# Kernel optimization log

Measured on AMD Instinct MI355X. Metric: run time of the kernel, lower is better.

The kernel has to match this reference:

```python
import jax, jax.numpy as jnp
import numpy as np

B, S, D, H, NS = 4, 4096, 1024, 16, 128
DA, DF = 512, 4096
DK, DV = DA // H, D // H  # 32, 64
TEMP = 1.0
EPS = 1e-6


def setup_inputs() -> dict:
    key = jax.random.key(0)
    ks = jax.random.split(key, 8)
    r = lambda k, shp: jax.random.normal(k, shp, jnp.float32) * 0.02
    return dict(
        x=jax.random.normal(ks[0], (B, S, D), jnp.float32),
        mask=jnp.ones((B, S), jnp.float32),
        residual_scale=jnp.ones((1,), jnp.float32),
        w_q=r(ks[1], (D, DA)), b_q=jnp.zeros((DA,), jnp.float32),
        w_kv=r(ks[2], (D, DA + D)), b_kv=jnp.zeros((DA + D,), jnp.float32),
        w_s=r(ks[3], (D, H * NS)), b_s=jnp.zeros((H * NS,), jnp.float32),
        w_cat=r(ks[4], (D, D)), b_cat=jnp.zeros((D,), jnp.float32),
        norm1_w=jnp.ones((D,), jnp.float32), norm2_w=jnp.ones((D,), jnp.float32),
        w1=r(ks[5], (D, DF)), b1=jnp.zeros((DF,), jnp.float32),
        w2=r(ks[6], (DF, D)), b2=jnp.zeros((D,), jnp.float32),
    )


def _rms(x, w):
    return x * jax.lax.rsqrt(jnp.mean(x * x, axis=-1, keepdims=True) + EPS) * w


def _forward(x, mask, residual_scale, w_q, b_q, w_kv, b_kv, w_s, b_s,
             w_cat, b_cat, norm1_w, norm2_w, w1, b1, w2, b2):
    neg = jnp.finfo(jnp.float32).min
    xn = _rms(x, norm1_w)
    q = (xn @ w_q + b_q).reshape(B, S, H, DK).transpose(0, 2, 1, 3)        # [B,H,S,DK]
    kv = (xn @ w_kv + b_kv).reshape(B, S, H, DK + DV).transpose(0, 2, 1, 3)  # [B,H,S,DK+DV]
    k_raw, v_raw = kv[..., :DK], kv[..., DK:]

    # DSZRC sampler: per-head soft routing of S tokens -> NS sampled KV rows
    logits = (x @ w_s + b_s).reshape(B, S, H, NS).transpose(0, 2, 3, 1)    # [B,H,NS,S]
    logits = jnp.where(mask[:, None, None, :] > 0, logits, neg)
    probs = jax.nn.softmax(logits / TEMP, axis=-1)
    kv_s = jnp.einsum('bhms,bhsd->bhmd', probs, kv)                        # [B,H,NS,DK+DV]
    k_s, v_s = kv_s[..., :DK], kv_s[..., DK:]

    # branch 1: dense SDPA over sampled KV
    scale = 1.0 / np.sqrt(DK).astype(np.float32)
    att = jax.nn.softmax(jnp.einsum('bhqd,bhkd->bhqk', q, k_s) * scale, axis=-1)
    out1 = jnp.einsum('bhqk,bhkd->bhqd', att, v_s)                         # [B,H,S,DV]

    # branch 2: fp16 sliding-window flash attn, left window = NS (keys i-NS..i)
    f16 = lambda t: t.astype(jnp.float16).astype(jnp.float32)
    qh, kh, vh = f16(q), f16(k_raw), f16(v_raw)
    bs = NS
    nb = S // bs
    qb = qh.reshape(B, H, nb, bs, DK)
    kb = kh.reshape(B, H, nb, bs, DK)
    vb = vh.reshape(B, H, nb, bs, DV)
    shift = lambda t: jnp.concatenate([jnp.zeros_like(t[:, :, :1]), t[:, :, :-1]], axis=2)
    kctx = jnp.concatenate([shift(kb), kb], axis=3)                        # [B,H,nb,2bs,DK]
    vctx = jnp.concatenate([shift(vb), vb], axis=3)
    sc = jnp.einsum('bhnad,bhnkd->bhnak', qb, kctx) * scale                # [B,H,nb,bs,2bs]
    a = jnp.arange(bs)[:, None]
    bcol = jnp.arange(2 * bs)[None, :]
    band = (bcol >= a) & (bcol <= a + NS)                                  # 0 <= q-k <= NS
    tpos = jnp.arange(nb)[:, None, None]
    valid = band[None] & ((tpos > 0) | (bcol >= bs)[None])                 # no keys before pos 0
    p = jax.nn.softmax(jnp.where(valid[None, None], sc, neg), axis=-1)
    out2 = f16(jnp.einsum('bhnak,bhnkd->bhnad', p, vctx)).reshape(B, H, S, DV)

    x_att = (out1 + out2).transpose(0, 2, 1, 3).reshape(B, S, D)
    x = x + (x_att @ w_cat + b_cat) * residual_scale
    h = _rms(x, norm2_w)
    x = x + (jax.nn.gelu(h @ w1 + b1, approximate=False) @ w2 + b2) * residual_scale
    return x


def reference(x, mask, residual_scale, w_q, b_q, w_kv, b_kv, w_s, b_s,
              w_cat, b_cat, norm1_w, norm2_w, w1, b1, w2, b2):
    return _forward(x, mask, residual_scale, w_q, b_q, w_kv, b_kv, w_s, b_s,
                    w_cat, b_cat, norm1_w, norm2_w, w1, b1, w2, b2)
```

## Files before the change

kernel.cpp:

```cpp
#include <hip/hip_runtime.h>
#include <cstdint>
#include <cmath>

#define DEV __device__ __forceinline__

using f16 = _Float16;
typedef f16  f16x4 __attribute__((ext_vector_type(4)));
typedef f16  f16x8 __attribute__((ext_vector_type(8)));
typedef float f32x4 __attribute__((ext_vector_type(4)));

constexpr int Bq = 4, Sq = 4096, Hq = 16;
constexpr int Tq = Bq * Sq;

DEV void gload_lds16(const void* g, void* l) {
  __builtin_amdgcn_global_load_lds(
      (const __attribute__((address_space(1))) void*)g,
      (__attribute__((address_space(3))) void*)l, 16, 0, 0);
}

DEV void stage_swz(const char* gbase, long gstride, char* lds, int nbytes,
                   int rowlog, int swzmask) {
  int tid = threadIdx.x;
  for (int b0 = 0; b0 < nbytes; b0 += 4096) {
    int P = b0 + tid * 16;
    int L = P ^ (((P >> rowlog) & swzmask) << 4);
    long row  = L >> rowlog;
    int  colb = L & ((1 << rowlog) - 1);
    gload_lds16(gbase + row * gstride + colb, lds + b0 + (tid & ~63) * 16);
  }
}

DEV void stage_swz512(const char* gbase, long gstride, char* lds, int nbytes,
                      int rowlog, int swzmask) {
  int tid = threadIdx.x;
  for (int b0 = 0; b0 < nbytes; b0 += 8192) {
    int P = b0 + tid * 16;
    int L = P ^ (((P >> rowlog) & swzmask) << 4);
    long row  = L >> rowlog;
    int  colb = L & ((1 << rowlog) - 1);
    gload_lds16(gbase + row * gstride + colb, lds + b0 + (tid & ~63) * 16);
  }
}

DEV float wave16_max(float v) {
#pragma unroll
  for (int d = 1; d < 16; d <<= 1) v = fmaxf(v, __shfl_xor(v, d, 64));
  return v;
}
DEV float wave16_sum(float v) {
#pragma unroll
  for (int d = 1; d < 16; d <<= 1) v += __shfl_xor(v, d, 64);
  return v;
}

__global__ __launch_bounds__(256) void wcast_k(const float* __restrict__ W,
                                               f16* __restrict__ Wt, int K, int N) {
  int n0 = blockIdx.x * 32, k0 = blockIdx.y * 32;
  __shared__ float tile[32][33];
  int tid = threadIdx.x, r = tid >> 5, c = tid & 31;
#pragma unroll
  for (int i = 0; i < 4; ++i)
    tile[r + i * 8][c] = W[(size_t)(k0 + r + i * 8) * N + n0 + c];
  __syncthreads();
#pragma unroll
  for (int i = 0; i < 4; ++i) {
    int rr = r + i * 8;
    Wt[(size_t)(n0 + rr) * K + k0 + c] = (f16)tile[c][rr];
  }
}

__global__ void bias_concat_k(const float* __restrict__ bq, const float* __restrict__ bkv,
                              float* __restrict__ out) {
  int i = blockIdx.x * 256 + threadIdx.x;
  out[i] = (i < 512) ? bq[i] : bkv[i - 512];
}

__global__ __launch_bounds__(256) void rmsnorm_k(const float* __restrict__ x,
                                                 const float* __restrict__ w,
                                                 f16* __restrict__ xn) {
  int row = blockIdx.x, tid = threadIdx.x;
  float4 v = ((const float4*)(x + (size_t)row * 1024))[tid];
  float ss = v.x * v.x + v.y * v.y + v.z * v.z + v.w * v.w;
#pragma unroll
  for (int d = 1; d < 64; d <<= 1) ss += __shfl_xor(ss, d, 64);
  __shared__ float red[4];
  if ((tid & 63) == 0) red[tid >> 6] = ss;
  __syncthreads();
  float tot = red[0] + red[1] + red[2] + red[3];
  float r = rsqrtf(tot * (1.0f / 1024.0f) + 1e-6f);
  float4 wv = ((const float4*)w)[tid];
  f16x4 o;
  o[0] = (f16)(v.x * r * wv.x); o[1] = (f16)(v.y * r * wv.y);
  o[2] = (f16)(v.z * r * wv.z); o[3] = (f16)(v.w * r * wv.w);
  *(f16x4*)(xn + (size_t)row * 1024 + tid * 4) = o;
}

template <int MODE>
__global__ __launch_bounds__(512) void gemm_k(const f16* __restrict__ A, const f16* __restrict__ Bt,
                                              const float* __restrict__ bias,
                                              float* __restrict__ outF, f16* __restrict__ o1,
                                              f16* __restrict__ o2, f16* __restrict__ o3,
                                              const float* __restrict__ resid,
                                              const float* __restrict__ rsp,
                                              int M, int N, int K, int lda, int ldb, int pp) {
  __shared__ alignas(16) char smA[32768];
  __shared__ alignas(16) char smB[32768];
  int nwgx = gridDim.x, nbc = gridDim.y;
  int bidl = blockIdx.y * nwgx + blockIdx.x;
  int cpx = (nwgx * nbc) >> 3;
  int xcd = bidl & 7, pos = bidl >> 3;
  int rpm = cpx / nbc;
  int nbi = pos / rpm, mbi = pos % rpm;
  int mb = xcd * rpm + mbi;
  long n0 = (long)nbi * 256;
  int tid = threadIdx.x, lane = tid & 63, wv = tid >> 6;
  int wr = wv >> 2, wc = wv & 3;
  long m0;
  long t0 = 0;
  int bq = 0;
  if (MODE == 5) {
    bq = mb >> 3; int sb = mb & 7;
    m0 = (long)sb * 256;
    t0 = (long)bq * 4096 + (long)pp * 2048 + m0;
  } else {
    m0 = (long)mb * 256;
  }
  f32x4 acc[8][4] = {};
  const char* Ab = (MODE == 5 || MODE == 7) ? nullptr : (const char*)(A + m0 * lda);
  const char* Bb = (const char*)(Bt + n0 * ldb);

  for (int k0 = 0; k0 < K; k0 += 64) {
    __syncthreads();
    stage_swz512(Bb + (long)k0 * 2, (long)ldb * 2, smB, 32768, 7, 7);
    if (MODE == 5) {
      int P = tid * 16;
#pragma unroll
      for (int b0 = 0; b0 < 32768; b0 += 8192) {
        int PP = b0 + P;
        int L = PP ^ (((PP >> 7) & 7) << 4);
        int row = L >> 7, colf = (L & 127) >> 1;
        const float* src = resid + (size_t)(t0 + row) * 1024 + k0 + colf;
        float4 u0 = *(const float4*)src;
        float4 u1 = *(const float4*)(src + 4);
        f16x8 o;
        o[0] = (f16)u0.x; o[1] = (f16)u0.y; o[2] = (f16)u0.z; o[3] = (f16)u0.w;
        o[4] = (f16)u1.x; o[5] = (f16)u1.y; o[6] = (f16)u1.z; o[7] = (f16)u1.w;
        *(f16x8*)(smA + PP) = o;
      }
    } else if (MODE == 7) {
      const char* Ab7 = (const char*)(A + (((m0 >> 12) * 16 + (k0 >> 6)) * 4096 + (m0 & 4095)) * 64);
      stage_swz512(Ab7, 128, smA, 32768, 7, 7);
    } else {
      stage_swz512(Ab + (long)k0 * 2, (long)lda * 2, smA, 32768, 7, 7);
    }
    __syncthreads();
#pragma unroll
    for (int kk = 0; kk < 2; ++kk) {
      int kbyte = kk * 64 + (lane >> 4) * 16;
      f16x8 aF[8], bF[4];
#pragma unroll
      for (int m = 0; m < 8; ++m) {
        int L = (wr * 128 + m * 16 + (lane & 15)) * 128 + kbyte;
        aF[m] = *(const f16x8*)(smA + (L ^ (((L >> 7) & 7) << 4)));
      }
#pragma unroll
      for (int n = 0; n < 4; ++n) {
        int L = (wc * 64 + n * 16 + (lane & 15)) * 128 + kbyte;
        bF[n] = *(const f16x8*)(smB + (L ^ (((L >> 7) & 7) << 4)));
      }
#pragma unroll
      for (int m = 0; m < 8; ++m)
#pragma unroll
        for (int n = 0; n < 4; ++n)
          acc[m][n] = __builtin_amdgcn_mfma_f32_16x16x32_f16(aF[m], bF[n], acc[m][n], 0, 0, 0);
    }
  }
  float rsv = (MODE == 2 || MODE == 7) ? rsp[0] : 0.f;
#pragma unroll
  for (int m = 0; m < 8; ++m)
#pragma unroll
    for (int n = 0; n < 4; ++n) {
      long gn = n0 + wc * 64 + n * 16 + (lane & 15);
      float bv = bias[gn];
      long rbase = m0 + wr * 128 + m * 16 + (lane >> 4) * 4;
      if (MODE == 4) {
        long b = rbase >> 12, s = rbase & 4095;
        if (gn < 512) {
          long h = gn >> 5, dk = gn & 31;
#pragma unroll
          for (int i = 0; i < 4; ++i)
            o1[(((size_t)b * 16 + h) * 4096 + s + i) * 32 + dk] = (f16)(acc[m][n][i] + bv);
        } else {
          long c2 = gn - 512, h = c2 / 96, j = c2 % 96;
          if (j < 32) {
#pragma unroll
            for (int i = 0; i < 4; ++i)
              o2[(((size_t)b * 16 + h) * 4096 + s + i) * 32 + j] = (f16)(acc[m][n][i] + bv);
          } else {
            f16x4 pk;
#pragma unroll
            for (int i = 0; i < 4; ++i) pk[i] = (f16)(acc[m][n][i] + bv);
            *(f16x4*)(o3 + (((size_t)b * 16 + h) * 64 + (j - 32)) * 4096 + s) = pk;
          }
        }
      } else {
#pragma unroll
        for (int i = 0; i < 4; ++i) {
          long gm = rbase + i;
          float v = acc[m][n][i] + bv;
          if (MODE == 2 || MODE == 7) {
            long idx = gm * N + gn;
            outF[idx] = resid[idx] + v * rsv;
          } else if (MODE == 3) {
            float u = v * 0.7978845608028654f * (1.f + 0.044715f * v * v);
            float e = __expf(fminf(2.f * u, 80.f));
            o1[gm * N + gn] = (f16)(v * (e / (e + 1.f)));
          } else {
            o1[((size_t)bq * 2048 + gn) * 2048 + gm] = (f16)v;
          }
        }
      }
    }
}

__global__ __launch_bounds__(256) void kvs_k(const f16* __restrict__ lt,
                                             const f16* __restrict__ kh,
                                             const f16* __restrict__ vT,
                                             const float* __restrict__ mask,
                                             float* __restrict__ pacc, int pass) {
  int gx = blockIdx.x, nsb = gx & 3, sc = gx >> 2;
  int h = blockIdx.y, b = blockIdx.z;
  int bh = b * 16 + h;
  __shared__ alignas(16) char smA[4096];
  __shared__ alignas(16) f16 smB[112][88];
  int tid = threadIdx.x, lane = tid & 63, w = tid >> 6;
  int mf = w >> 1, nb0 = (w & 1) * 4, nfr = (w & 1) ? 3 : 4;
  for (int idx = tid; idx < 16 * 64; idx += 256) {
    int r = 96 + (idx >> 6), c2 = idx & 63;
    smB[r][c2] = (r == 96) ? (f16)1.0f : (f16)0.0f;
  }
  f32x4 acc[4] = {};
  const f16* ltb = lt + ((size_t)bh * 128 + nsb * 32) * 2048;
  for (int it = 0; it < 4; ++it) {
    int sl0 = sc * 256 + it * 64;
    int s0g = pass * 2048 + sl0;
    __syncthreads();
    {
      int P = tid * 16;
      int L = P ^ (((P >> 7) & 7) << 4);
      int row = L >> 7, colf = (L & 127) >> 1;
      f16x8 lv = *(const f16x8*)(ltb + (size_t)row * 2048 + sl0 + colf);
      const float* mrow = mask + (size_t)b * 4096 + s0g + colf;
      float4 m0v = *(const float4*)mrow, m1v = *(const float4*)(mrow + 4);
      float mm[8] = {m0v.x, m0v.y, m0v.z, m0v.w, m1v.x, m1v.y, m1v.z, m1v.w};
      f16x8 o;
#pragma unroll
      for (int j = 0; j < 8; ++j)
        o[j] = (f16)((mm[j] > 0.f) ? expf((float)lv[j] - 8.0f) : 0.0f);
      *(f16x8*)(smA + P) = o;
    }
    {
      int sl = tid >> 2, jg = (tid & 3) * 8;
      f16x8 u = *(const f16x8*)(kh + ((size_t)bh * 4096 + s0g + sl) * 32 + jg);
#pragma unroll
      for (int j = 0; j < 8; ++j) smB[jg + j][sl] = u[j];
    }
#pragma unroll
    for (int half = 0; half < 2; ++half) {
      int task = tid + half * 256;
      int dv = task >> 3, sl0v = (task & 7) * 8;
      f16x8 u = *(const f16x8*)(vT + ((size_t)bh * 64 + dv) * 4096 + s0g + sl0v);
      *(f16x8*)(&smB[32 + dv][sl0v]) = u;
    }
    __syncthreads();
#pragma unroll
    for (int kk = 0; kk < 2; ++kk) {
      int kbyte = kk * 64 + (lane >> 4) * 16;
      int L = (mf * 16 + (lane & 15)) * 128 + kbyte;
      f16x8 aF = *(const f16x8*)(smA + (L ^ (((L >> 7) & 7) << 4)));
#pragma unroll
      for (int n = 0; n < 4; ++n)
        if (n < nfr) {
          f16x8 bF = *(const f16x8*)((const char*)smB + ((nb0 + n) * 16 + (lane & 15)) * 176 + kbyte);
          acc[n] = __builtin_amdgcn_mfma_f32_16x16x32_f16(aF, bF, acc[n], 0, 0, 0);
        }
    }
  }
  int slot = pass * 8 + sc;
  float* pb = pacc + (((size_t)bh * 4 + nsb) * 16 + slot) * 3584;
#pragma unroll
  for (int n = 0; n < 4; ++n)
    if (n < nfr) {
      int col = (nb0 + n) * 16 + (lane & 15);
#pragma unroll
      for (int i = 0; i < 4; ++i) {
        int nsrow = mf * 16 + (lane >> 4) * 4 + i;
        pb[(size_t)nsrow * 112 + col] = acc[n][i];
      }
    }
}

__global__ __launch_bounds__(256) void kvs_fin_k(const float* __restrict__ pacc,
                                                 f16* __restrict__ ks, f16* __restrict__ vst) {
  int bh = blockIdx.x, tid = threadIdx.x;
  __shared__ float den[128];
  const float* base = pacc + (size_t)bh * 4 * 16 * 3584;
  if (tid < 128) {
    int nsb = tid >> 5, nsl = tid & 31;
    float d = 0.f;
#pragma unroll
    for (int slot = 0; slot < 16; ++slot)
      d += base[((size_t)nsb * 16 + slot) * 3584 + (size_t)nsl * 112 + 96];
    den[tid] = d;
  }
  __syncthreads();
  for (int e = tid; e < 12288; e += 256) {
    int ns = e / 96, j = e % 96;
    int nsb = ns >> 5, nsl = ns & 31;
    float sv = 0.f;
#pragma unroll
    for (int slot = 0; slot < 16; ++slot)
      sv += base[((size_t)nsb * 16 + slot) * 3584 + (size_t)nsl * 112 + j];
    float v = sv / den[ns];
    if (j < 32) ks[((size_t)bh * 128 + ns) * 32 + j] = (f16)v;
    else        vst[((size_t)bh * 64 + (j - 32)) * 128 + ns] = (f16)v;
  }
}

__global__ __launch_bounds__(256) void att_k(const f16* __restrict__ qh,
                                             const f16* __restrict__ kh,
                                             const f16* __restrict__ vTh,
                                             const f16* __restrict__ ksb,
                                             const f16* __restrict__ vstb,
                                             f16* __restrict__ xatt) {
  int ntj = blockIdx.x, h = blockIdx.y, b = blockIdx.z;
  int nt = ((ntj & 7) << 3) | (ntj >> 3);
  int bh = b * 16 + h, s0 = nt * 64;
  __shared__ alignas(16) char smQ[4096];
  __shared__ alignas(16) char smK[4096];
  __shared__ alignas(16) char smV[8192];
  __shared__ alignas(16) f16 smP[4][16][72];
  int tid = threadIdx.x, lane = tid & 63, w = tid >> 6;
  const float scale = 0.17677669529663687f;
  stage_swz((const char*)(qh + ((size_t)bh * 4096 + s0) * 32), 64, smQ, 4096, 6, 3);

  float mrun[4], lrun[4], m1[4], l1[4];
#pragma unroll
  for (int i = 0; i < 4; ++i) { mrun[i] = -1e30f; lrun[i] = 0.f; m1[i] = -1e30f; l1[i] = 0.f; }
  f32x4 o2[4] = {}, o1[4] = {};

  for (int c = 0; c < 5; ++c) {
    bool win = (c < 3);
    long kb = (long)s0 + (c - 2) * 64;
    if (win && kb < 0) continue;
    __syncthreads();
    if (win) {
      stage_swz((const char*)(kh + ((size_t)bh * 4096 + kb) * 32), 64, smK, 4096, 6, 3);
      stage_swz((const char*)(vTh + (size_t)bh * 64 * 4096 + kb), 8192, smV, 8192, 7, 7);
    } else {
      int sc = c - 3;
      stage_swz((const char*)(ksb + ((size_t)bh * 128 + sc * 64) * 32), 64, smK, 4096, 6, 3);
      stage_swz((const char*)(vstb + (size_t)bh * 64 * 128 + sc * 64), 256, smV, 8192, 7, 7);
    }
    __syncthreads();
    f32x4 s[4] = {};
    {
      int kbyte = (lane >> 4) * 16;
      int Lq = (w * 16 + (lane & 15)) * 64 + kbyte;
      f16x8 aF = *(const f16x8*)(smQ + (Lq ^ (((Lq >> 6) & 3) << 4)));
#pragma unroll
      for (int n = 0; n < 4; ++n) {
        int Lk = (n * 16 + (lane & 15)) * 64 + kbyte;
        f16x8 bF = *(const f16x8*)(smK + (Lk ^ (((Lk >> 6) & 3) << 4)));
        s[n] = __builtin_amdgcn_mfma_f32_16x16x32_f16(aF, bF, s[n], 0, 0, 0);
      }
    }
    float* mr = win ? mrun : m1;
    float* lr = win ? lrun : l1;
    f32x4* oo = win ? o2 : o1;
#pragma unroll
    for (int i = 0; i < 4; ++i) {
      int a2 = w * 16 + (lane >> 4) * 4 + i;
      float nm = mr[i];
#pragma unroll
      for (int n = 0; n < 4; ++n) {
        int kl = n * 16 + (lane & 15);
        bool valid = !win || (c == 1) || (c == 0 ? (kl >= a2) : (kl <= a2));
        float v = valid ? s[n][i] * scale : -1e30f;
        s[n][i] = v; nm = fmaxf(nm, v);
      }
      nm = wave16_max(nm);
      float alpha = expf(mr[i] - nm);
      float sum = 0.f;
#pragma unroll
      for (int n = 0; n < 4; ++n) { float p = expf(s[n][i] - nm); s[n][i] = p; sum += p; }
      sum = wave16_sum(sum);
      lr[i] = lr[i] * alpha + sum;
      mr[i] = nm;
#pragma unroll
      for (int n = 0; n < 4; ++n) oo[n][i] *= alpha;
    }
#pragma unroll
    for (int n = 0; n < 4; ++n)
#pragma unroll
      for (int i = 0; i < 4; ++i)
        smP[w][(lane >> 4) * 4 + i][n * 16 + (lane & 15)] = (f16)s[n][i];
#pragma unroll
    for (int kk = 0; kk < 2; ++kk) {
      int kb2 = kk * 64 + (lane >> 4) * 16;
      f16x8 aP = *(const f16x8*)((const char*)smP[w] + (lane & 15) * 144 + kb2);
#pragma unroll
      for (int n = 0; n < 4; ++n) {
        int dv = n * 16 + (lane & 15);
        int Lv = dv * 128 + kb2;
        f16x8 bV = *(const f16x8*)(smV + (Lv ^ (((Lv >> 7) & 7) << 4)));
        oo[n] = __builtin_amdgcn_mfma_f32_16x16x32_f16(aP, bV, oo[n], 0, 0, 0);
      }
    }
  }
  f16* xb = xatt + ((size_t)bh * 4096 + s0) * 64;
#pragma unroll
  for (int n = 0; n < 4; ++n)
#pragma unroll
    for (int i = 0; i < 4; ++i) {
      int row = w * 16 + (lane >> 4) * 4 + i, dv = n * 16 + (lane & 15);
      xb[(size_t)row * 64 + dv] = (f16)(o2[n][i] / lrun[i] + o1[n][i] / l1[i]);
    }
}

__global__ void sentinel_k(float* out, size_t n, float val) {
  size_t i = (size_t)blockIdx.x * 256 + threadIdx.x;
  size_t stride = (size_t)gridDim.x * 256;
  for (; i < n; i += stride) out[i] = val;
}

constexpr size_t OFF_WQKV = 0;
constexpr size_t OFF_WSC  = OFF_WQKV + 2048ull * 1024 * 2;
constexpr size_t OFF_WCAT = OFF_WSC  + 2048ull * 1024 * 2;
constexpr size_t OFF_W1   = OFF_WCAT + 1024ull * 1024 * 2;
constexpr size_t OFF_W2   = OFF_W1   + 4096ull * 1024 * 2;
constexpr size_t OFF_BQKV = OFF_W2   + 1024ull * 4096 * 2;
constexpr size_t OFF_ZB   = OFF_BQKV + 8192;
constexpr size_t OFF_Q    = OFF_ZB   + 4096;
constexpr size_t OFF_K    = OFF_Q    + (size_t)Tq * 512 * 2;
constexpr size_t OFF_P1   = OFF_K    + (size_t)Tq * 512 * 2;
constexpr size_t OFF_VT   = OFF_P1   + (size_t)Tq * 1024 * 2;
constexpr size_t OFF_KVA  = OFF_VT   + (size_t)Tq * 1024 * 2;
constexpr size_t OFF_KS   = OFF_KVA  + 64ull * 128 * 112 * 4;
constexpr size_t OFF_VST  = OFF_KS   + 64ull * 128 * 32 * 2;
constexpr size_t WS_NEED  = OFF_VST  + 64ull * 64 * 128 * 2;

extern "C" void kernel_launch(void* const* d_in, const int* in_sizes, int n_in,
                              void* d_out, int out_size, void* d_ws, size_t ws_size,
                              hipStream_t stream) {
  float* xo = (float*)d_out;
  if (ws_size < WS_NEED) {
    float val = -(1000.0f + (float)(ws_size / 1000000ull));
    sentinel_k<<<2048, 256, 0, stream>>>(xo, (size_t)out_size, val);
    return;
  }
  const float* x     = (const float*)d_in[0];
  const float* mask  = (const float*)d_in[1];
  const float* rsp   = (const float*)d_in[2];
  const float* w_q   = (const float*)d_in[3];
  const float* b_q   = (const float*)d_in[4];
  const float* w_kv  = (const float*)d_in[5];
  const float* b_kv  = (const float*)d_in[6];
  const float* w_s   = (const float*)d_in[7];
  const float* b_s   = (const float*)d_in[8];
  const float* w_cat = (const float*)d_in[9];
  const float* b_cat = (const float*)d_in[10];
  const float* n1w   = (const float*)d_in[11];
  const float* n2w   = (const float*)d_in[12];
  const float* w1    = (const float*)d_in[13];
  const float* b1    = (const float*)d_in[14];
  const float* w2    = (const float*)d_in[15];
  const float* b2    = (const float*)d_in[16];
  char* ws = (char*)d_ws;

  f16*   wqkv_t = (f16*)(ws + OFF_WQKV);
  f16*   ws_t   = (f16*)(ws + OFF_WSC);
  f16*   wcat_t = (f16*)(ws + OFF_WCAT);
  f16*   w1_t   = (f16*)(ws + OFF_W1);
  f16*   w2_t   = (f16*)(ws + OFF_W2);
  float* bqkv   = (float*)(ws + OFF_BQKV);
  f16*   q_h    = (f16*)(ws + OFF_Q);
  f16*   k_h    = (f16*)(ws + OFF_K);
  f16*   h_h    = (f16*)(ws + OFF_Q);
  f16*   xn_h   = (f16*)(ws + OFF_P1);
  f16*   lt16   = (f16*)(ws + OFF_P1);
  f16*   xatt_h = (f16*)(ws + OFF_P1);
  f16*   g_h    = (f16*)(ws + OFF_P1);
  f16*   vT_h   = (f16*)(ws + OFF_VT);
  f16*   ks_h   = (f16*)(ws + OFF_KS);
  f16*   vst_h  = (f16*)(ws + OFF_VST);

  wcast_k<<<dim3(16, 32),  256, 0, stream>>>(w_q,   wqkv_t,              1024, 512);
  wcast_k<<<dim3(48, 32),  256, 0, stream>>>(w_kv,  wqkv_t + 512 * 1024, 1024, 1536);
  wcast_k<<<dim3(64, 32),  256, 0, stream>>>(w_s,   ws_t,                1024, 2048);
  wcast_k<<<dim3(32, 32),  256, 0, stream>>>(w_cat, wcat_t,              1024, 1024);
  wcast_k<<<dim3(128, 32), 256, 0, stream>>>(w1,    w1_t,                1024, 4096);
  wcast_k<<<dim3(32, 128), 256, 0, stream>>>(w2,    w2_t,                4096, 1024);
  bias_concat_k<<<8, 256, 0, stream>>>(b_q, b_kv, bqkv);

  rmsnorm_k<<<Tq, 256, 0, stream>>>(x, n1w, xn_h);
  gemm_k<4><<<dim3(64, 8), 512, 0, stream>>>(xn_h, wqkv_t, bqkv, nullptr, q_h, k_h, vT_h,
                                             nullptr, nullptr, Tq, 2048, 1024, 1024, 1024, 0);
  for (int p = 0; p < 2; ++p) {
    gemm_k<5><<<dim3(32, 8), 512, 0, stream>>>(nullptr, ws_t, b_s, nullptr, lt16, nullptr, nullptr,
                                               x, nullptr, 8192, 2048, 1024, 0, 1024, p);
    kvs_k<<<dim3(32, 16, 4), 256, 0, stream>>>(lt16, k_h, vT_h, mask, xo, p);
  }
  kvs_fin_k<<<64, 256, 0, stream>>>(xo, ks_h, vst_h);
  att_k<<<dim3(64, 16, 4), 256, 0, stream>>>(q_h, k_h, vT_h, ks_h, vst_h, xatt_h);
  gemm_k<7><<<dim3(64, 4), 512, 0, stream>>>(xatt_h, wcat_t, b_cat, xo, nullptr, nullptr, nullptr,
                                             x, rsp, Tq, 1024, 1024, 0, 1024, 0);
  rmsnorm_k<<<Tq, 256, 0, stream>>>(xo, n2w, h_h);
  for (int mc = 0; mc < 2; ++mc) {
    const f16* hA = h_h + (size_t)mc * 8192 * 1024;
    float* xoc = xo + (size_t)mc * 8192 * 1024;
    gemm_k<3><<<dim3(32, 16), 512, 0, stream>>>(hA, w1_t, b1, nullptr, g_h, nullptr, nullptr,
                                                nullptr, nullptr, 8192, 4096, 1024, 1024, 1024, 0);
    gemm_k<2><<<dim3(32, 4), 512, 0, stream>>>(g_h, w2_t, b2, xoc, nullptr, nullptr, nullptr,
                                               xoc, rsp, 8192, 1024, 4096, 4096, 4096, 0);
  }
}
```

Measured before the change: 1.065 ms.

## Double-buffer GEMM LDS staging and use 128x128 tiles for residual GEMMs

Adds double-buffered LDS in all GEMMs so the next K-tile is prefetched while MFMAs run on the current one, leaving one barrier per iteration. The residual-output GEMMs (w_cat and w2) move to a new 128x128, 256-thread kernel so they launch more workgroups on N=1024 and fill the CUs better. The 256x256 kernel now uses 128KB of LDS, which limits occupancy to one workgroup per CU.

Result: faster. 924.4 us (-13.2%).

```diff
diff --git a/kernel.cpp b/kernel.cpp
--- a/kernel.cpp
+++ b/kernel.cpp
@@ -96,15 +96,93 @@
 }
 
 template <int MODE>
-__global__ __launch_bounds__(512) void gemm_k(const f16* __restrict__ A, const f16* __restrict__ Bt,
+__global__ __launch_bounds__(256) void gemm_k(const f16* __restrict__ A, const f16* __restrict__ Bt,
                                               const float* __restrict__ bias,
-                                              float* __restrict__ outF, f16* __restrict__ o1,
-                                              f16* __restrict__ o2, f16* __restrict__ o3,
+                                              float* __restrict__ outF,
                                               const float* __restrict__ resid,
                                               const float* __restrict__ rsp,
-                                              int M, int N, int K, int lda, int ldb, int pp) {
-  __shared__ alignas(16) char smA[32768];
-  __shared__ alignas(16) char smB[32768];
+                                              int M, int N, int K, int lda, int ldb) {
+  __shared__ alignas(16) char smA[2][16384];
+  __shared__ alignas(16) char smB[2][16384];
+  int nwgx = gridDim.x, nbc = gridDim.y;
+  int bidl = blockIdx.y * nwgx + blockIdx.x;
+  int cpx = (nwgx * nbc) >> 3;
+  int xcd = bidl & 7, pos = bidl >> 3;
+  int rpm = cpx / nbc;
+  int nbi = pos / rpm, mbi = pos % rpm;
+  int mb = xcd * rpm + mbi;
+  long n0 = (long)nbi * 128;
+  int tid = threadIdx.x, lane = tid & 63, wv = tid >> 6, wr = wv >> 1, wc = wv & 1;
+  long m0 = (long)mb * 128;
+  f32x4 acc[4][4] = {};
+  const char* Ab = (MODE == 7) ? nullptr : (const char*)(A + m0 * lda);
+  const char* Bb = (const char*)(Bt + n0 * ldb);
+
+  auto stageAB = [&](int buf, int k0) {
+    stage_swz(Bb + (long)k0 * 2, (long)ldb * 2, smB[buf], 16384, 7, 7);
+    if (MODE == 7) {
+      const char* Ab7 = (const char*)(A + (((m0 >> 12) * 16 + (k0 >> 6)) * 4096 + (m0 & 4095)) * 64);
+      stage_swz(Ab7, 128, smA[buf], 16384, 7, 7);
+    } else {
+      stage_swz(Ab + (long)k0 * 2, (long)lda * 2, smA[buf], 16384, 7, 7);
+    }
+  };
+
+  stageAB(0, 0);
+  __syncthreads();
+  int cur = 0;
+  for (int k0 = 0; k0 < K; k0 += 64) {
+    if (k0 + 64 < K) stageAB(cur ^ 1, k0 + 64);
+#pragma unroll
+    for (int kk = 0; kk < 2; ++kk) {
+      int kbyte = kk * 64 + (lane >> 4) * 16;
+      f16x8 aF[4], bF[4];
+#pragma unroll
+      for (int m = 0; m < 4; ++m) {
+        int L = (wr * 64 + m * 16 + (lane & 15)) * 128 + kbyte;
+        aF[m] = *(const f16x8*)(smA[cur] + (L ^ (((L >> 7) & 7) << 4)));
+      }
+#pragma unroll
+      for (int n = 0; n < 4; ++n) {
+        int L = (wc * 64 + n * 16 + (lane & 15)) * 128 + kbyte;
+        bF[n] = *(const f16x8*)(smB[cur] + (L ^ (((L >> 7) & 7) << 4)));
+      }
+#pragma unroll
+      for (int m = 0; m < 4; ++m)
+#pragma unroll
+        for (int n = 0; n < 4; ++n)
+          acc[m][n] = __builtin_amdgcn_mfma_f32_16x16x32_f16(aF[m], bF[n], acc[m][n], 0, 0, 0);
+    }
+    __syncthreads();
+    cur ^= 1;
+  }
+  float rsv = rsp[0];
+#pragma unroll
+  for (int m = 0; m < 4; ++m)
+#pragma unroll
+    for (int n = 0; n < 4; ++n) {
+      long gn = n0 + wc * 64 + n * 16 + (lane & 15);
+      float bv = bias[gn];
+      long rbase = m0 + wr * 64 + m * 16 + (lane >> 4) * 4;
+#pragma unroll
+      for (int i = 0; i < 4; ++i) {
+        long gm = rbase + i;
+        float v = acc[m][n][i] + bv;
+        long idx = gm * N + gn;
+        outF[idx] = resid[idx] + v * rsv;
+      }
+    }
+}
+
+template <int MODE>
+__global__ __launch_bounds__(512) void gemm256_k(const f16* __restrict__ A, const f16* __restrict__ Bt,
+                                                 const float* __restrict__ bias,
+                                                 f16* __restrict__ o1, f16* __restrict__ o2,
+                                                 f16* __restrict__ o3,
+                                                 const float* __restrict__ resid,
+                                                 int M, int N, int K, int lda, int ldb, int pp) {
+  __shared__ alignas(16) char smA[2][32768];
+  __shared__ alignas(16) char smB[2][32768];
   int nwgx = gridDim.x, nbc = gridDim.y;
   int bidl = blockIdx.y * nwgx + blockIdx.x;
   int cpx = (nwgx * nbc) >> 3;
@@ -126,12 +204,11 @@
     m0 = (long)mb * 256;
   }
   f32x4 acc[8][4] = {};
-  const char* Ab = (MODE == 5 || MODE == 7) ? nullptr : (const char*)(A + m0 * lda);
+  const char* Ab = (MODE == 5) ? nullptr : (const char*)(A + m0 * lda);
   const char* Bb = (const char*)(Bt + n0 * ldb);
 
-  for (int k0 = 0; k0 < K; k0 += 64) {
-    __syncthreads();
-    stage_swz512(Bb + (long)k0 * 2, (long)ldb * 2, smB, 32768, 7, 7);
+  auto stageAB = [&](int buf, int k0) {
+    stage_swz512(Bb + (long)k0 * 2, (long)ldb * 2, smB[buf], 32768, 7, 7);
     if (MODE == 5) {
       int P = tid * 16;
 #pragma unroll
@@ -145,15 +222,18 @@
         f16x8 o;
         o[0] = (f16)u0.x; o[1] = (f16)u0.y; o[2] = (f16)u0.z; o[3] = (f16)u0.w;
         o[4] = (f16)u1.x; o[5] = (f16)u1.y; o[6] = (f16)u1.z; o[7] = (f16)u1.w;
-        *(f16x8*)(smA + PP) = o;
-      }
-    } else if (MODE == 7) {
-      const char* Ab7 = (const char*)(A + (((m0 >> 12) * 16 + (k0 >> 6)) * 4096 + (m0 & 4095)) * 64);
-      stage_swz512(Ab7, 128, smA, 32768, 7, 7);
+        *(f16x8*)(smA[buf] + PP) = o;
+      }
     } else {
-      stage_swz512(Ab + (long)k0 * 2, (long)lda * 2, smA, 32768, 7, 7);
-    }
-    __syncthreads();
+      stage_swz512(Ab + (long)k0 * 2, (long)lda * 2, smA[buf], 32768, 7, 7);
+    }
+  };
+
+  stageAB(0, 0);
+  __syncthreads();
+  int cur = 0;
+  for (int k0 = 0; k0 < K; k0 += 64) {
+    if (k0 + 64 < K) stageAB(cur ^ 1, k0 + 64);
 #pragma unroll
     for (int kk = 0; kk < 2; ++kk) {
       int kbyte = kk * 64 + (lane >> 4) * 16;
@@ -161,12 +241,12 @@
 #pragma unroll
       for (int m = 0; m < 8; ++m) {
         int L = (wr * 128 + m * 16 + (lane & 15)) * 128 + kbyte;
-        aF[m] = *(const f16x8*)(smA + (L ^ (((L >> 7) & 7) << 4)));
+        aF[m] = *(const f16x8*)(smA[cur] + (L ^ (((L >> 7) & 7) << 4)));
       }
 #pragma unroll
       for (int n = 0; n < 4; ++n) {
         int L = (wc * 64 + n * 16 + (lane & 15)) * 128 + kbyte;
-        bF[n] = *(const f16x8*)(smB + (L ^ (((L >> 7) & 7) << 4)));
+        bF[n] = *(const f16x8*)(smB[cur] + (L ^ (((L >> 7) & 7) << 4)));
       }
 #pragma unroll
       for (int m = 0; m < 8; ++m)
@@ -174,8 +254,9 @@
         for (int n = 0; n < 4; ++n)
           acc[m][n] = __builtin_amdgcn_mfma_f32_16x16x32_f16(aF[m], bF[n], acc[m][n], 0, 0, 0);
     }
-  }
-  float rsv = (MODE == 2 || MODE == 7) ? rsp[0] : 0.f;
+    __syncthreads();
+    cur ^= 1;
+  }
 #pragma unroll
   for (int m = 0; m < 8; ++m)
 #pragma unroll
@@ -208,10 +289,7 @@
         for (int i = 0; i < 4; ++i) {
           long gm = rbase + i;
           float v = acc[m][n][i] + bv;
-          if (MODE == 2 || MODE == 7) {
-            long idx = gm * N + gn;
-            outF[idx] = resid[idx] + v * rsv;
-          } else if (MODE == 3) {
+          if (MODE == 3) {
             float u = v * 0.7978845608028654f * (1.f + 0.044715f * v * v);
             float e = __expf(fminf(2.f * u, 80.f));
             o1[gm * N + gn] = (f16)(v * (e / (e + 1.f)));
@@ -504,24 +582,24 @@
   bias_concat_k<<<8, 256, 0, stream>>>(b_q, b_kv, bqkv);
 
   rmsnorm_k<<<Tq, 256, 0, stream>>>(x, n1w, xn_h);
-  gemm_k<4><<<dim3(64, 8), 512, 0, stream>>>(xn_h, wqkv_t, bqkv, nullptr, q_h, k_h, vT_h,
-                                             nullptr, nullptr, Tq, 2048, 1024, 1024, 1024, 0);
+  gemm256_k<4><<<dim3(64, 8), 512, 0, stream>>>(xn_h, wqkv_t, bqkv, q_h, k_h, vT_h,
+                                                nullptr, Tq, 2048, 1024, 1024, 1024, 0);
   for (int p = 0; p < 2; ++p) {
-    gemm_k<5><<<dim3(32, 8), 512, 0, stream>>>(nullptr, ws_t, b_s, nullptr, lt16, nullptr, nullptr,
-                                               x, nullptr, 8192, 2048, 1024, 0, 1024, p);
+    gemm256_k<5><<<dim3(32, 8), 512, 0, stream>>>(nullptr, ws_t, b_s, lt16, nullptr, nullptr,
+                                                  x, 8192, 2048, 1024, 0, 1024, p);
     kvs_k<<<dim3(32, 16, 4), 256, 0, stream>>>(lt16, k_h, vT_h, mask, xo, p);
   }
   kvs_fin_k<<<64, 256, 0, stream>>>(xo, ks_h, vst_h);
   att_k<<<dim3(64, 16, 4), 256, 0, stream>>>(q_h, k_h, vT_h, ks_h, vst_h, xatt_h);
-  gemm_k<7><<<dim3(64, 4), 512, 0, stream>>>(xatt_h, wcat_t, b_cat, xo, nullptr, nullptr, nullptr,
-                                             x, rsp, Tq, 1024, 1024, 0, 1024, 0);
+  gemm_k<7><<<dim3(128, 8), 256, 0, stream>>>(xatt_h, wcat_t, b_cat, xo,
+                                              x, rsp, Tq, 1024, 1024, 0, 1024);
   rmsnorm_k<<<Tq, 256, 0, stream>>>(xo, n2w, h_h);
   for (int mc = 0; mc < 2; ++mc) {
     const f16* hA = h_h + (size_t)mc * 8192 * 1024;
     float* xoc = xo + (size_t)mc * 8192 * 1024;
-    gemm_k<3><<<dim3(32, 16), 512, 0, stream>>>(hA, w1_t, b1, nullptr, g_h, nullptr, nullptr,
-                                                nullptr, nullptr, 8192, 4096, 1024, 1024, 1024, 0);
-    gemm_k<2><<<dim3(32, 4), 512, 0, stream>>>(g_h, w2_t, b2, xoc, nullptr, nullptr, nullptr,
-                                               xoc, rsp, 8192, 1024, 4096, 4096, 4096, 0);
-  }
-}
+    gemm256_k<3><<<dim3(32, 16), 512, 0, stream>>>(hA, w1_t, b1, g_h, nullptr, nullptr,
+                                                   nullptr, 8192, 4096, 1024, 1024, 1024, 0);
+    gemm_k<2><<<dim3(64, 8), 256, 0, stream>>>(g_h, w2_t, b2, xoc,
+                                               xoc, rsp, 8192, 1024, 4096, 4096, 4096);
+  }
+}
```
